# Optimization experiments

Measured on AMD Instinct MI355X. Metric: run time of the kernel, lower is better.

Reference implementation:

```python
import jax, jax.numpy as jnp
import numpy as np

E = 384      # EMBEDDING_SIZE
DFF = 1536
H = 6        # NUM_HEADS
D = E // H   # ATTN_DIM_SIZE = 64
T = 256      # SEQ_LEN
L = 6        # NUM_BLOCKS
V = 65       # VOCAB_SIZE
NPOS = 10000.0
B = 128


def _pos_encoding():
    i = jnp.arange(T, dtype=jnp.float32)[:, None]
    k = jnp.arange(E // 2, dtype=jnp.float32)[None, :]
    ang = i / jnp.power(NPOS, 2.0 * k / E)   # [T, E/2]
    pe = jnp.zeros((T, E), dtype=jnp.float32)
    pe = pe.at[:, 0::2].set(jnp.sin(ang))
    pe = pe.at[:, 1::2].set(jnp.cos(ang))
    return pe


def setup_inputs() -> dict:
    key = jax.random.key(0)
    ks = jax.random.split(key, 24)
    s = 0.02
    n = lambda k, shp: (jax.random.normal(k, shp, dtype=jnp.float32) * s)
    inp = {
        'tokens': jax.random.randint(ks[0], (B, T), 0, V),
        'pos_enc': _pos_encoding(),
        'emb': n(ks[1], (V, E)),
        # stacked per-layer params [L, ...]; weights stored as (in, out)
        'Wq': n(ks[2], (L, E, E)), 'bq': jnp.zeros((L, E)),
        'Wk': n(ks[3], (L, E, E)), 'bk': jnp.zeros((L, E)),
        'Wv': n(ks[4], (L, E, E)), 'bv': jnp.zeros((L, E)),
        'Wo': n(ks[5], (L, E, E)), 'bo': jnp.zeros((L, E)),
        'ln1_g': jnp.ones((L, E)), 'ln1_b': jnp.zeros((L, E)),
        'W1': n(ks[6], (L, E, DFF)), 'c1': jnp.zeros((L, DFF)),
        'W2': n(ks[7], (L, DFF, E)), 'c2': jnp.zeros((L, E)),
        'ln2_g': jnp.ones((L, E)), 'ln2_b': jnp.zeros((L, E)),
        'Wl': n(ks[8], (E, V)), 'bl': jnp.zeros((V,)),
    }
    return inp


def _layer_norm(x, g, b, eps=1e-5):
    mu = jnp.mean(x, axis=-1, keepdims=True)
    var = jnp.mean((x - mu) ** 2, axis=-1, keepdims=True)
    return (x - mu) * jax.lax.rsqrt(var + eps) * g + b


def _decoder(tokens, pos_enc, emb, Wq, bq, Wk, bk, Wv, bv, Wo, bo,
             ln1_g, ln1_b, W1, c1, W2, c2, ln2_g, ln2_b, Wl, bl):
    b_, t_ = tokens.shape
    x = emb[tokens] + pos_enc[None, :t_, :]            # [B,T,E]
    causal = jnp.tril(jnp.ones((t_, t_), dtype=bool)) # tril mask
    scale = D ** (-0.5)

    def block(x, p):
        (wq, bq_, wk, bk_, wv, bv_, wo, bo_, g1, be1, w1, c1_, w2, c2_, g2, be2) = p
        h = _layer_norm(x, g1, be1)
        q = (h @ wq + bq_).reshape(b_, t_, H, D)
        k = (h @ wk + bk_).reshape(b_, t_, H, D)
        v = (h @ wv + bv_).reshape(b_, t_, H, D)
        scores = jnp.einsum('bqhd,bkhd->bhqk', q, k) * scale
        scores = jnp.where(causal[None, None], scores, -jnp.inf)
        attn = jax.nn.softmax(scores, axis=-1)
        o = jnp.einsum('bhqk,bkhd->bqhd', attn, v).reshape(b_, t_, E)
        x = x + (o @ wo + bo_)
        h2 = _layer_norm(x, g2, be2)
        x = x + (jax.nn.relu(h2 @ w1 + c1_) @ w2 + c2_)
        return x, None

    params = (Wq, bq, Wk, bk, Wv, bv, Wo, bo, ln1_g, ln1_b, W1, c1, W2, c2, ln2_g, ln2_b)
    x, _ = jax.lax.scan(block, x, params)
    return x @ Wl + bl                                 # [B,T,V]


def reference(tokens, pos_enc, emb, Wq, bq, Wk, bk, Wv, bv, Wo, bo,
              ln1_g, ln1_b, W1, c1, W2, c2, ln2_g, ln2_b, Wl, bl):
    return _decoder(tokens, pos_enc, emb, Wq, bq, Wk, bk, Wv, bv, Wo, bo,
                    ln1_g, ln1_b, W1, c1, W2, c2, ln2_g, ln2_b, Wl, bl)
```

## Files before the change

kernel.cpp:

```cpp
#include <hip/hip_runtime.h>
#include <hip/hip_bf16.h>
#include <stdint.h>

constexpr int E   = 384;
constexpr int DFF = 1536;
constexpr int NH  = 6;
constexpr int HD  = 64;
constexpr int T   = 256;
constexpr int NL  = 6;
constexpr int NV  = 65;
constexpr int BB  = 128;
constexpr int MTOT = BB * T;
constexpr int CB  = 32;

typedef __bf16 bf16;
typedef __attribute__((ext_vector_type(8))) __bf16 bf16x8;
typedef __attribute__((ext_vector_type(4))) __bf16 bf16x4;
typedef __attribute__((ext_vector_type(4))) float floatx4;

__device__ __forceinline__ void gload_lds16(const void* g, void* l) {
    __builtin_amdgcn_global_load_lds(
        (const __attribute__((address_space(1))) void*)g,
        (__attribute__((address_space(3))) void*)l, 16, 0, 0);
}

#define GBN 128

template <int MODE, int SWAP, int W>
__device__ __forceinline__ void gemm_body(
    char* AsB,
    const bf16* __restrict__ A, int lda,
    const bf16* __restrict__ Bf,
    const float* __restrict__ bias,
    void* __restrict__ Cv, void* __restrict__ Cv2, int ldc,
    int nt, int mt, int Nvalid, int K, int relu)
{
    constexpr int BM   = W * 32;
    constexpr int ABUF = BM * 64;

    int tid = threadIdx.x;
    int lane = tid & 63;
    int wid = tid >> 6;
    int wr = wid >> 1, wc = wid & 1;
    int lq = lane >> 4, lr = lane & 15;

    const bf16* Ab = A + (long)mt * BM * lda;

    int rp0 = wid * 8 + (lane >> 3);
    int s   = lane & 7;
    int sp  = s ^ (rp0 & 7);
    int rowA = 2 * rp0 + (sp >> 2);
    int kOff = (sp & 3) * 8;
    const bf16* srcA0 = Ab + (long)rowA * lda + kOff;
    const bf16* srcA1 = srcA0 + (long)(BM / 2) * lda;
    int dst0 = wid * 1024;
    int dst1 = W * 1024 + wid * 1024;

    int nks = K / 32;
    const bf16* Bq = Bf + ((long)(nt * 8 + wc * 4) * nks) * 512 + lane * 8;

    floatx4 acc[4][4];
#pragma unroll
    for (int i = 0; i < 4; i++)
#pragma unroll
        for (int j = 0; j < 4; j++) acc[i][j] = floatx4{0.f, 0.f, 0.f, 0.f};

    int afo = (wr * 32 + (lr >> 1)) * 128 +
              (((((lr & 1) << 2) | lq) ^ (lr >> 1)) << 4);

    gload_lds16(srcA0, AsB + dst0);
    gload_lds16(srcA1, AsB + dst1);
    if (nks > 1) {
        gload_lds16(srcA0 + 32, AsB + ABUF + dst0);
        gload_lds16(srcA1 + 32, AsB + ABUF + dst1);
        asm volatile("s_waitcnt vmcnt(2)" ::: "memory");
    } else {
        asm volatile("s_waitcnt vmcnt(0)" ::: "memory");
    }
    __builtin_amdgcn_s_barrier();

    int o0 = 0, o1 = ABUF, o2 = 2 * ABUF;
    for (int ki = 0; ki < nks; ++ki) {
        bf16x8 bb[4];
#pragma unroll
        for (int ni = 0; ni < 4; ni++)
            bb[ni] = *(const bf16x8*)(Bq + ((long)ni * nks + ki) * 512);
        __builtin_amdgcn_sched_barrier(0);
        if (ki + 2 < nks) {
            long ko = (long)(ki + 2) * 32;
            gload_lds16(srcA0 + ko, AsB + o2 + dst0);
            gload_lds16(srcA1 + ko, AsB + o2 + dst1);
        }
        const char* rp = AsB + o0 + afo;
        bf16x8 af[4];
#pragma unroll
        for (int mi = 0; mi < 4; mi++)
            af[mi] = *(const bf16x8*)(rp + mi * 1024);
        __builtin_amdgcn_s_setprio(1);
#pragma unroll
        for (int mi = 0; mi < 4; mi++)
#pragma unroll
            for (int ni = 0; ni < 4; ni++)
                acc[mi][ni] = SWAP
                    ? __builtin_amdgcn_mfma_f32_16x16x32_bf16(bb[ni], af[mi], acc[mi][ni], 0, 0, 0)
                    : __builtin_amdgcn_mfma_f32_16x16x32_bf16(af[mi], bb[ni], acc[mi][ni], 0, 0, 0);
        __builtin_amdgcn_s_setprio(0);
        if (ki + 1 < nks) {
            if (ki + 2 < nks)
                asm volatile("s_waitcnt vmcnt(2) lgkmcnt(0)" ::: "memory");
            else
                asm volatile("s_waitcnt vmcnt(0) lgkmcnt(0)" ::: "memory");
            __builtin_amdgcn_s_barrier();
        }
        int t = o0; o0 = o1; o1 = o2; o2 = t;
    }

    int m0 = mt * BM, n0 = nt * GBN;
#pragma unroll
    for (int mi = 0; mi < 4; mi++) {
#pragma unroll
        for (int ni = 0; ni < 4; ni++) {
            floatx4 v = acc[mi][ni];
            if (SWAP) {
                int rowL = m0 + wr * 64 + mi * 16 + lr;
                int col0 = n0 + wc * 64 + ni * 16 + lq * 4;
                if (MODE == 5) {
                    bf16x4 pv;
#pragma unroll
                    for (int r = 0; r < 4; r++) pv[r] = (bf16)(v[r] + bias[col0 + r]);
                    *(bf16x4*)((bf16*)Cv + (long)rowL * 768 + col0) = pv;
                } else if (MODE == 1) {
                    bf16* Cp = (bf16*)Cv;
                    bf16x4* ptr = (bf16x4*)(Cp + (long)rowL * ldc + col0);
                    bf16x4 old = *ptr;
                    bf16x4 pv;
#pragma unroll
                    for (int r = 0; r < 4; r++)
                        pv[r] = (bf16)((float)old[r] + v[r] + bias[col0 + r]);
                    *ptr = pv;
                } else if (MODE == 4) {
                    float* Cp = (float*)Cv;
#pragma unroll
                    for (int r = 0; r < 4; r++)
                        if (col0 + r < Nvalid)
                            Cp[(long)rowL * ldc + col0 + r] = v[r] + bias[col0 + r];
                } else {
                    if (col0 < Nvalid) {
                        bf16x4 pv;
#pragma unroll
                        for (int r = 0; r < 4; r++) {
                            float x = v[r] + (bias ? bias[col0 + r] : 0.f);
                            if (relu) x = fmaxf(x, 0.f);
                            pv[r] = (bf16)x;
                        }
                        *(bf16x4*)((bf16*)Cv + (long)rowL * ldc + col0) = pv;
                    }
                }
            } else {
                int row0 = m0 + wr * 64 + mi * 16 + lq * 4;
                int colL = n0 + wc * 64 + ni * 16 + lr;
                float bv = bias[colL];
                bf16x4 pv;
#pragma unroll
                for (int r = 0; r < 4; r++) pv[r] = (bf16)(v[r] + bv);
                int bidx = row0 >> 8, pos = row0 & 255, e = colL - 768;
                *(bf16x4*)((bf16*)Cv2 + (long)bidx * (E * T) + (long)e * T + pos) = pv;
            }
        }
    }
}

template <int MODE, int W>
__global__ __launch_bounds__(W * 64, 4) void k_gemm(
    const bf16* __restrict__ A, int lda,
    const bf16* __restrict__ Bf,
    const float* __restrict__ bias,
    void* __restrict__ Cv, void* __restrict__ Cv2, int ldc,
    int Mtiles, int Ntiles, int Nvalid, int K,
    int relu)
{
    __shared__ __align__(16) char AsB[3 * W * 32 * 64];

    int nb = gridDim.x;
    int per = nb >> 3;
    int bphys = blockIdx.x;
    int bid = (bphys & 7) * per + (bphys >> 3);

    int nt = bid % Ntiles;
    int mt = bid / Ntiles;

    if (MODE == 5 && nt >= 6)
        gemm_body<5, 0, W>(AsB, A, lda, Bf, bias, Cv, Cv2, ldc, nt, mt, Nvalid, K, relu);
    else
        gemm_body<MODE, 1, W>(AsB, A, lda, Bf, bias, Cv, Cv2, ldc, nt, mt, Nvalid, K, relu);
}

__global__ __launch_bounds__(256) void k_attn(
    const bf16* __restrict__ qk, const bf16* __restrict__ vt,
    bf16* __restrict__ o)
{
    int nb = gridDim.x;
    int per = nb >> 3;
    int bphys = blockIdx.x;
    int bid = (bphys & 7) * per + (bphys >> 3);

    int qt = bid & 3; bid >>= 2;
    int h = bid % NH; int b = bid / NH;
    int tid = threadIdx.x;
    int lane = tid & 63;
    int w = tid >> 6;
    int lq = lane >> 4;
    int lr = lane & 15;

    __shared__ __align__(16) bf16 Ks[256 * 72];
    __shared__ __align__(16) bf16 Vs[64 * 264];

    const bf16* qbase = qk + (long)(b * T + qt * 64 + w * 16) * 768 + h * 64;
    const bf16* kbase = qk + (long)(b * T) * 768 + 384 + h * 64;
    const bf16* vbase = vt + ((long)b * E + h * 64) * T;

#pragma unroll
    for (int i = 0; i < 8; i++) {
        int idx = i * 256 + tid;
        int row = idx >> 3, off = (idx & 7) * 8;
        *(bf16x8*)(&Ks[row * 72 + off]) = *(const bf16x8*)(kbase + (long)row * 768 + off);
    }
#pragma unroll
    for (int i = 0; i < 8; i++) {
        int idx = i * 256 + tid;
        int row = idx >> 5, off = (idx & 31) * 8;
        *(bf16x8*)(&Vs[row * 264 + off]) = *(const bf16x8*)(vbase + (long)row * 256 + off);
    }

    bf16x8 aq0 = *(const bf16x8*)(qbase + (long)lr * 768 + lq * 8);
    bf16x8 aq1 = *(const bf16x8*)(qbase + (long)lr * 768 + 32 + lq * 8);

    __syncthreads();

    const int ntmax = qt * 4 + 3;
    floatx4 zero = {0.f, 0.f, 0.f, 0.f};
    floatx4 s[16];
#pragma unroll
    for (int nt = 0; nt < 16; nt++) s[nt] = zero;

#pragma unroll
    for (int nt = 0; nt < 16; nt++) {
        if (nt <= ntmax) {
            const bf16* kp = &Ks[(nt * 16 + lr) * 72 + lq * 8];
            bf16x8 b0 = *(const bf16x8*)(kp);
            bf16x8 b1 = *(const bf16x8*)(kp + 32);
            s[nt] = __builtin_amdgcn_mfma_f32_16x16x32_bf16(aq0, b0, s[nt], 0, 0, 0);
            s[nt] = __builtin_amdgcn_mfma_f32_16x16x32_bf16(aq1, b1, s[nt], 0, 0, 0);
        }
    }

    int trow0 = qt * 64 + w * 16 + lq * 4;
    float m4[4] = {-3e38f, -3e38f, -3e38f, -3e38f};
#pragma unroll
    for (int nt = 0; nt < 16; nt++) {
        if (nt <= ntmax) {
            int tc = nt * 16 + lr;
#pragma unroll
            for (int r = 0; r < 4; r++) {
                float v = s[nt][r] * 0.125f;
                if (tc > trow0 + r) v = -3e38f;
                s[nt][r] = v;
                m4[r] = fmaxf(m4[r], v);
            }
        }
    }
#pragma unroll
    for (int r = 0; r < 4; r++) {
#pragma unroll
        for (int off = 1; off < 16; off <<= 1)
            m4[r] = fmaxf(m4[r], __shfl_xor(m4[r], off, 64));
    }

    float l4[4] = {0.f, 0.f, 0.f, 0.f};
#pragma unroll
    for (int nt = 0; nt < 16; nt++) {
        if (nt <= ntmax) {
#pragma unroll
            for (int r = 0; r < 4; r++) {
                float pv = __expf(s[nt][r] - m4[r]);
                l4[r] += pv;
                s[nt][r] = pv;
            }
        }
    }
#pragma unroll
    for (int r = 0; r < 4; r++) {
#pragma unroll
        for (int off = 1; off < 16; off <<= 1)
            l4[r] += __shfl_xor(l4[r], off, 64);
    }

    __syncthreads();

    bf16* P = Ks + w * (16 * 264);
#pragma unroll
    for (int nt = 0; nt < 16; nt++) {
        if (nt <= ntmax) {
#pragma unroll
            for (int r = 0; r < 4; r++)
                P[(lq * 4 + r) * 264 + nt * 16 + lr] = (bf16)s[nt][r];
        }
    }

    floatx4 oacc[4];
#pragma unroll
    for (int nd = 0; nd < 4; nd++) oacc[nd] = zero;
    const int kkmax = 2 * (qt + 1);
#pragma unroll
    for (int kk = 0; kk < 8; kk++) {
        if (kk < kkmax) {
            bf16x8 ap = *(const bf16x8*)(&P[lr * 264 + kk * 32 + lq * 8]);
#pragma unroll
            for (int nd = 0; nd < 4; nd++) {
                bf16x8 bv = *(const bf16x8*)(&Vs[(nd * 16 + lr) * 264 + kk * 32 + lq * 8]);
                oacc[nd] = __builtin_amdgcn_mfma_f32_16x16x32_bf16(ap, bv, oacc[nd], 0, 0, 0);
            }
        }
    }

#pragma unroll
    for (int r = 0; r < 4; r++) {
        float inv = 1.0f / l4[r];
        long rowg = (long)b * T + trow0 + r;
#pragma unroll
        for (int nd = 0; nd < 4; nd++) {
            o[rowg * E + h * 64 + nd * 16 + lr] = (bf16)(oacc[nd][r] * inv);
        }
    }
}

__global__ void k_ln(const bf16* __restrict__ x, const float* __restrict__ g,
                     const float* __restrict__ b, bf16* __restrict__ h) {
    int row = blockIdx.x * 4 + (threadIdx.x >> 6);
    int lane = threadIdx.x & 63;
    const bf16* xr = x + (long)row * E;
    float v[6];
    float s = 0.f;
#pragma unroll
    for (int i = 0; i < 6; i++) { v[i] = (float)xr[lane + 64 * i]; s += v[i]; }
#pragma unroll
    for (int o = 1; o < 64; o <<= 1) s += __shfl_xor(s, o, 64);
    float mu = s * (1.0f / E);
    float q = 0.f;
#pragma unroll
    for (int i = 0; i < 6; i++) { float d = v[i] - mu; q += d * d; }
#pragma unroll
    for (int o = 1; o < 64; o <<= 1) q += __shfl_xor(q, o, 64);
    float rs = rsqrtf(q * (1.0f / E) + 1e-5f);
    bf16* hr = h + (long)row * E;
#pragma unroll
    for (int i = 0; i < 6; i++) {
        int c = lane + 64 * i;
        hr[c] = (bf16)((v[i] - mu) * rs * g[c] + b[c]);
    }
}

__global__ void k_transpose_frag(const float* __restrict__ W, bf16* __restrict__ Wf,
                                 int K, int N, int NPAD) {
    long idx = (long)blockIdx.x * 256 + threadIdx.x;
    long per = (long)NPAD * K;
    int l = (int)(idx / per);
    long r = idx - (long)l * per;
    int j = (int)(r & 7); r >>= 3;
    int lane = (int)(r & 63); r >>= 6;
    int nks = K / 32;
    int ks = (int)(r % nks);
    int c16 = (int)(r / nks);
    int col = c16 * 16 + (lane & 15);
    int k = ks * 32 + (lane >> 4) * 8 + j;
    Wf[idx] = (col < N) ? (bf16)W[((long)l * K + k) * N + col] : (bf16)0.0f;
}

__global__ void k_transpose_qkv_frag(const float* __restrict__ Wq, const float* __restrict__ Wk,
                                     const float* __restrict__ Wv, bf16* __restrict__ Wf) {
    long idx = (long)blockIdx.x * 256 + threadIdx.x;
    long per = (long)1152 * E;
    int l = (int)(idx / per);
    long r = idx - (long)l * per;
    int j = (int)(r & 7); r >>= 3;
    int lane = (int)(r & 63); r >>= 6;
    int nks = E / 32;
    int ks = (int)(r % nks);
    int c16 = (int)(r / nks);
    int col = c16 * 16 + (lane & 15);
    int k = ks * 32 + (lane >> 4) * 8 + j;
    const float* src;
    int cc;
    if (col < 384)      { src = Wq; cc = col; }
    else if (col < 768) { src = Wk; cc = col - 384; }
    else                { src = Wv; cc = col - 768; }
    Wf[idx] = (bf16)src[((long)l * E + k) * E + cc];
}

__global__ void k_bias_qkv(const float* __restrict__ bq, const float* __restrict__ bk,
                           const float* __restrict__ bv, float* __restrict__ bqkv) {
    int idx = blockIdx.x * 256 + threadIdx.x;
    int l = idx / 1152;
    int j = idx - l * 1152;
    const float* src;
    int jj;
    if (j < 384)      { src = bq; jj = j; }
    else if (j < 768) { src = bk; jj = j - 384; }
    else              { src = bv; jj = j - 768; }
    bqkv[idx] = src[l * E + jj];
}

__global__ void k_embed(const int* __restrict__ tokens, const float* __restrict__ pos,
                        const float* __restrict__ emb, bf16* __restrict__ x) {
    long idx = (long)blockIdx.x * 256 + threadIdx.x;
    int e = (int)(idx % E);
    long bt = idx / E;
    int t = (int)(bt % T);
    int tok = tokens[bt];
    x[idx] = (bf16)(emb[(long)tok * E + e] + pos[(long)t * E + e]);
}

extern "C" void kernel_launch(void* const* d_in, const int* in_sizes, int n_in,
                              void* d_out, int out_size, void* d_ws, size_t ws_size,
                              hipStream_t stream) {
    const int*   tokens = (const int*)d_in[0];
    const float* pos  = (const float*)d_in[1];
    const float* emb  = (const float*)d_in[2];
    const float* Wq   = (const float*)d_in[3];
    const float* bq   = (const float*)d_in[4];
    const float* Wk   = (const float*)d_in[5];
    const float* bk   = (const float*)d_in[6];
    const float* Wv   = (const float*)d_in[7];
    const float* bv   = (const float*)d_in[8];
    const float* Wo   = (const float*)d_in[9];
    const float* bo   = (const float*)d_in[10];
    const float* g1   = (const float*)d_in[11];
    const float* be1  = (const float*)d_in[12];
    const float* W1   = (const float*)d_in[13];
    const float* c1   = (const float*)d_in[14];
    const float* W2   = (const float*)d_in[15];
    const float* c2   = (const float*)d_in[16];
    const float* g2   = (const float*)d_in[17];
    const float* be2  = (const float*)d_in[18];
    const float* Wl   = (const float*)d_in[19];
    const float* bl   = (const float*)d_in[20];

    char* p = (char*)d_ws;
    bf16* x  = (bf16*)p;   p += (long)MTOT * E * 2;
    bf16* h  = (bf16*)p;   p += (long)MTOT * E * 2;
    bf16* qk = (bf16*)p;   p += (long)MTOT * 768 * 2;
    bf16* vt = (bf16*)p;   p += (long)BB * E * T * 2;
    bf16* SP = (bf16*)p;   p += (long)CB * NH * T * T * 2;
    bf16* WqkvF = (bf16*)p; p += (long)NL * 1152 * E * 2;
    bf16* WoF = (bf16*)p;  p += (long)NL * E * E * 2;
    bf16* W1F = (bf16*)p;  p += (long)NL * DFF * E * 2;
    bf16* W2F = (bf16*)p;  p += (long)NL * E * DFF * 2;
    bf16* WlF = (bf16*)p;  p += (long)128 * E * 2;
    float* bqkv = (float*)p; p += (long)NL * 1152 * 4;
    bf16* mid = qk;
    bf16* o   = h;
    (void)SP;

    k_transpose_qkv_frag<<<(NL * 1152 * E) / 256, 256, 0, stream>>>(Wq, Wk, Wv, WqkvF);
    k_transpose_frag<<<(NL * E * E) / 256, 256, 0, stream>>>(Wo, WoF, E, E, E);
    k_transpose_frag<<<(NL * DFF * E) / 256, 256, 0, stream>>>(W1, W1F, E, DFF, DFF);
    k_transpose_frag<<<(NL * E * DFF) / 256, 256, 0, stream>>>(W2, W2F, DFF, E, E);
    k_transpose_frag<<<(128 * E) / 256, 256, 0, stream>>>(Wl, WlF, E, NV, 128);
    k_bias_qkv<<<(NL * 1152) / 256, 256, 0, stream>>>(bq, bk, bv, bqkv);

    k_embed<<<(MTOT * E) / 256, 256, 0, stream>>>(tokens, pos, emb, x);

    for (int l = 0; l < NL; l++) {
        k_ln<<<MTOT / 4, 256, 0, stream>>>(x, g1 + l * E, be1 + l * E, h);
        k_gemm<5, 8><<<128 * 9, 512, 0, stream>>>(h, E, WqkvF + (long)l * 1152 * E,
                                                  bqkv + l * 1152, qk, vt, 0,
                                                  128, 9, 1152, E, 0);
        k_attn<<<BB * NH * 4, 256, 0, stream>>>(qk, vt, o);
        k_gemm<1, 4><<<256 * 3, 256, 0, stream>>>(o, E, WoF + (long)l * E * E,
                                                  bo + l * E, x, nullptr, E,
                                                  256, 3, E, E, 0);
        k_ln<<<MTOT / 4, 256, 0, stream>>>(x, g2 + l * E, be2 + l * E, h);
        k_gemm<0, 8><<<128 * 12, 512, 0, stream>>>(h, E, W1F + (long)l * DFF * E,
                                                   c1 + l * DFF, mid, nullptr, DFF,
                                                   128, 12, DFF, E, 1);
        k_gemm<1, 4><<<256 * 3, 256, 0, stream>>>(mid, DFF, W2F + (long)l * E * DFF,
                                                  c2 + l * E, x, nullptr, E,
                                                  256, 3, E, DFF, 0);
    }

    k_gemm<4, 4><<<256 * 1, 256, 0, stream>>>(x, E, WlF,
                                              bl, d_out, nullptr, NV,
                                              256, 1, NV, E, 0);
}
```

Measured before the change: 1.814 ms.

## Stage B weight fragments through LDS with async global_load_lds pipeline

Previously each wave loaded its B (weight) fragments straight from global memory into registers every k-step, so the waves sharing a column block fetched the same data redundantly and the MFMA loop waited on global latency. Now the B tile is copied into the triple-buffered LDS stage together with A using global_load_lds, and the fragments are read back from LDS. This puts B loads inside the same prefetch pipeline as A, two steps ahead. The cost is larger LDS usage per block, which may lower occupancy, and extra LDS read traffic.

```diff
diff --git a/kernel.cpp b/kernel.cpp
--- a/kernel.cpp
+++ b/kernel.cpp
@@ -35,8 +35,9 @@
     void* __restrict__ Cv, void* __restrict__ Cv2, int ldc,
     int nt, int mt, int Nvalid, int K, int relu)
 {
-    constexpr int BM   = W * 32;
-    constexpr int ABUF = BM * 64;
+    constexpr int BM     = W * 32;
+    constexpr int ABYTES = BM * 64;
+    constexpr int SBUF   = ABYTES + 8192;
 
     int tid = threadIdx.x;
     int lane = tid & 63;
@@ -57,7 +58,19 @@
     int dst1 = W * 1024 + wid * 1024;
 
     int nks = K / 32;
-    const bf16* Bq = Bf + ((long)(nt * 8 + wc * 4) * nks) * 512 + lane * 8;
+
+    const bf16* srcB0;
+    const bf16* srcB1 = nullptr;
+    int dstB0, dstB1 = 0;
+    if constexpr (W == 8) {
+        srcB0 = Bf + ((long)(nt * 8 + wid) * nks) * 512 + lane * 8;
+        dstB0 = ABYTES + wid * 1024;
+    } else {
+        srcB0 = Bf + ((long)(nt * 8 + wid * 2) * nks) * 512 + lane * 8;
+        srcB1 = Bf + ((long)(nt * 8 + wid * 2 + 1) * nks) * 512 + lane * 8;
+        dstB0 = ABYTES + (wid * 2) * 1024;
+        dstB1 = ABYTES + (wid * 2 + 1) * 1024;
+    }
 
     floatx4 acc[4][4];
 #pragma unroll
@@ -67,49 +80,64 @@
 
     int afo = (wr * 32 + (lr >> 1)) * 128 +
               (((((lr & 1) << 2) | lq) ^ (lr >> 1)) << 4);
-
-    gload_lds16(srcA0, AsB + dst0);
-    gload_lds16(srcA1, AsB + dst1);
+    int bfo = ABYTES + wc * 4096 + lane * 16;
+
+    auto stage = [&](int ks, int bo) {
+        long ka = (long)ks * 32;
+        gload_lds16(srcA0 + ka, AsB + bo + dst0);
+        gload_lds16(srcA1 + ka, AsB + bo + dst1);
+        long kb = (long)ks * 512;
+        gload_lds16(srcB0 + kb, AsB + bo + dstB0);
+        if constexpr (W == 4)
+            gload_lds16(srcB1 + kb, AsB + bo + dstB1);
+    };
+
+    int o0 = 0, o1 = SBUF, o2 = 2 * SBUF;
+
+    stage(0, o0);
     if (nks > 1) {
-        gload_lds16(srcA0 + 32, AsB + ABUF + dst0);
-        gload_lds16(srcA1 + 32, AsB + ABUF + dst1);
-        asm volatile("s_waitcnt vmcnt(2)" ::: "memory");
+        stage(1, o1);
+        if constexpr (W == 8)
+            asm volatile("s_waitcnt vmcnt(3)" ::: "memory");
+        else
+            asm volatile("s_waitcnt vmcnt(4)" ::: "memory");
     } else {
         asm volatile("s_waitcnt vmcnt(0)" ::: "memory");
     }
     __builtin_amdgcn_s_barrier();
 
-    int o0 = 0, o1 = ABUF, o2 = 2 * ABUF;
     for (int ki = 0; ki < nks; ++ki) {
-        bf16x8 bb[4];
+        if (ki + 2 < nks) stage(ki + 2, o2);
+        __builtin_amdgcn_sched_barrier(0);
+
+        bf16x8 bfr[4];
 #pragma unroll
         for (int ni = 0; ni < 4; ni++)
-            bb[ni] = *(const bf16x8*)(Bq + ((long)ni * nks + ki) * 512);
-        __builtin_amdgcn_sched_barrier(0);
-        if (ki + 2 < nks) {
-            long ko = (long)(ki + 2) * 32;
-            gload_lds16(srcA0 + ko, AsB + o2 + dst0);
-            gload_lds16(srcA1 + ko, AsB + o2 + dst1);
-        }
-        const char* rp = AsB + o0 + afo;
+            bfr[ni] = *(const bf16x8*)(AsB + o0 + bfo + ni * 1024);
         bf16x8 af[4];
 #pragma unroll
         for (int mi = 0; mi < 4; mi++)
-            af[mi] = *(const bf16x8*)(rp + mi * 1024);
+            af[mi] = *(const bf16x8*)(AsB + o0 + afo + mi * 1024);
+
         __builtin_amdgcn_s_setprio(1);
 #pragma unroll
         for (int mi = 0; mi < 4; mi++)
 #pragma unroll
             for (int ni = 0; ni < 4; ni++)
                 acc[mi][ni] = SWAP
-                    ? __builtin_amdgcn_mfma_f32_16x16x32_bf16(bb[ni], af[mi], acc[mi][ni], 0, 0, 0)
-                    : __builtin_amdgcn_mfma_f32_16x16x32_bf16(af[mi], bb[ni], acc[mi][ni], 0, 0, 0);
+                    ? __builtin_amdgcn_mfma_f32_16x16x32_bf16(bfr[ni], af[mi], acc[mi][ni], 0, 0, 0)
+                    : __builtin_amdgcn_mfma_f32_16x16x32_bf16(af[mi], bfr[ni], acc[mi][ni], 0, 0, 0);
         __builtin_amdgcn_s_setprio(0);
+
         if (ki + 1 < nks) {
-            if (ki + 2 < nks)
-                asm volatile("s_waitcnt vmcnt(2) lgkmcnt(0)" ::: "memory");
-            else
+            if (ki + 2 < nks) {
+                if constexpr (W == 8)
+                    asm volatile("s_waitcnt vmcnt(3) lgkmcnt(0)" ::: "memory");
+                else
+                    asm volatile("s_waitcnt vmcnt(4) lgkmcnt(0)" ::: "memory");
+            } else {
                 asm volatile("s_waitcnt vmcnt(0) lgkmcnt(0)" ::: "memory");
+            }
             __builtin_amdgcn_s_barrier();
         }
         int t = o0; o0 = o1; o1 = o2; o2 = t;
@@ -179,7 +207,7 @@
     int Mtiles, int Ntiles, int Nvalid, int K,
     int relu)
 {
-    __shared__ __align__(16) char AsB[3 * W * 32 * 64];
+    __shared__ __align__(16) char AsB[3 * (W * 32 * 64 + 8192)];
 
     int nb = gridDim.x;
     int per = nb >> 3;
```

After: 1.701 ms. 1.07x faster.
